# Kernel optimization log

Measured on AMD Instinct MI355X. Metric: run time of the kernel, lower is better.

## Reference

```python
import jax, jax.numpy as jnp
import numpy as np

NEG_SLOPE = 0.2  # PyG GATConv default leaky_relu slope


def add_self_loops(edge_index, n):
    loop = jnp.arange(n, dtype=edge_index.dtype)
    return jnp.concatenate([edge_index, jnp.stack([loop, loop])], axis=1)


def gat_conv(x, edge_index, W, a_src, a_dst, b):
    """PyG-style GATConv: x [N,Cin], W [Cin,H*F], a_* [H,F], b [H*F]. Returns [N,H*F]."""
    N = x.shape[0]
    H, F = a_src.shape
    xw = (x @ W).reshape(N, H, F)                      # per-head projected features
    alpha_s = jnp.sum(xw * a_src, axis=-1)             # [N,H]
    alpha_d = jnp.sum(xw * a_dst, axis=-1)             # [N,H]
    src, dst = edge_index[0], edge_index[1]
    e = alpha_s[src] + alpha_d[dst]                    # [E,H]
    e = jnp.where(e > 0, e, NEG_SLOPE * e)             # leaky_relu
    # segment softmax over edges grouped by destination node
    emax = jax.ops.segment_max(e, dst, num_segments=N)
    emax = jnp.where(jnp.isfinite(emax), emax, 0.0)
    p = jnp.exp(e - emax[dst])
    denom = jax.ops.segment_sum(p, dst, num_segments=N)
    alpha = p / (denom[dst] + 1e-16)                   # [E,H]
    msg = xw[src] * alpha[:, :, None]                  # [E,H,F]
    out = jax.ops.segment_sum(msg, dst, num_segments=N)  # [N,H,F]
    return out.reshape(N, H * F) + b


def setup_inputs() -> dict:
    key = jax.random.key(0)
    ks = jax.random.split(key, 10)
    N, E, FEAT, HID, HEADS = 50000, 800000, 256, 64, 4
    x = jax.random.normal(ks[0], (N, FEAT), dtype=jnp.float32)
    src = jax.random.randint(ks[1], (E,), 0, N, dtype=jnp.int64)
    dst = jax.random.randint(ks[2], (E,), 0, N, dtype=jnp.int64)
    dst = jnp.where(src == dst, (dst + 1) % N, dst)  # no pre-existing self loops
    edge_index = jnp.stack([src, dst])
    s1 = 1.0 / np.sqrt(FEAT)
    s2 = 1.0 / np.sqrt(HID * HEADS)
    return {
        "x": x,
        "edge_index": edge_index,
        "w1": jax.random.normal(ks[3], (FEAT, HEADS * HID), dtype=jnp.float32) * s1,
        "a_src1": jax.random.normal(ks[4], (HEADS, HID), dtype=jnp.float32) * 0.1,
        "a_dst1": jax.random.normal(ks[5], (HEADS, HID), dtype=jnp.float32) * 0.1,
        "b1": jnp.zeros((HEADS * HID,), dtype=jnp.float32),
        "w2": jax.random.normal(ks[6], (HEADS * HID, 1), dtype=jnp.float32) * s2,
        "a_src2": jax.random.normal(ks[7], (1, 1), dtype=jnp.float32) * 0.1,
        "a_dst2": jax.random.normal(ks[8], (1, 1), dtype=jnp.float32) * 0.1,
        "b2": jnp.zeros((1,), dtype=jnp.float32),
    }


def reference(x, edge_index, w1, a_src1, a_dst1, b1, w2, a_src2, a_dst2, b2):
    N = x.shape[0]
    ei = add_self_loops(edge_index, N)
    h = gat_conv(x, ei, w1, a_src1, a_dst1, b1)
    h = jax.nn.relu(h)  # dropout is identity in eval mode
    return gat_conv(h, ei, w2, a_src2, a_dst2, b2)
```

## Files before the change

kernel.cpp:

```cpp
#include <hip/hip_runtime.h>
#include <cstdint>
#include <cstddef>

#define NEG_SLOPE 0.2f
#define CAP 64

typedef _Float16 f16x4 __attribute__((ext_vector_type(4)));
typedef _Float16 f16x8 __attribute__((ext_vector_type(8)));
typedef float    f32x4 __attribute__((ext_vector_type(4)));

static __device__ __forceinline__ float leaky(float x){ return x > 0.f ? x : NEG_SLOPE*x; }
static __device__ __forceinline__ unsigned fkey(float f){
  unsigned u = __float_as_uint(f);
  return (u & 0x80000000u) ? ~u : (u | 0x80000000u);
}
static __device__ __forceinline__ float fdecode(unsigned k){
  return __uint_as_float((k & 0x80000000u) ? (k ^ 0x80000000u) : ~k);
}

__global__ __launch_bounds__(256) void k_setup(const unsigned int* __restrict__ w, int E,
                                               int* __restrict__ flag, unsigned* __restrict__ gkey,
                                               const float* __restrict__ W, _Float16* __restrict__ Bp,
                                               int* __restrict__ cnt, int N){
  int bid = blockIdx.x, tid = threadIdx.x;
  if (bid == 0){
    __shared__ int s;
    if (tid == 0) s = 0;
    if (tid < 8) gkey[tid] = 0u;
    __syncthreads();
    int nz = 0;
    long long total = 2LL * E;
    #pragma unroll
    for (int j = 0; j < 8; ++j){
      long long idx = ((long long)(tid * 8 + j) * total) / 2048;
      idx |= 1;
      if (idx < total) nz |= (w[idx] != 0u);
    }
    if (__any(nz) && (tid & 63) == 0) atomicOr(&s, 1);
    __syncthreads();
    if (tid == 0) *flag = s;
  } else if (bid <= 256){
    int c = bid - 1;
    int k = tid;
    float v = W[k*256 + c];
    int nb   = c >> 4;
    int frow = c & 15;
    int ks   = k >> 5;
    int kg   = (k >> 3) & 3;
    int ke   = k & 7;
    size_t idx = ((size_t)((nb*8 + ks)*64 + kg*16 + frow) << 3) + ke;
    Bp[idx] = (_Float16)v;
  } else {
    int base = (bid - 257)*1024 + tid*4;
    #pragma unroll
    for (int j = 0; j < 4; ++j){
      int idx = base + j;
      if (idx < N) cnt[idx] = 0;
    }
  }
}

__global__ __launch_bounds__(256) void k_gemm_scatter(const float* __restrict__ A,
                                                      const _Float16* __restrict__ Bp,
                                                      const float* __restrict__ a_src,
                                                      const float* __restrict__ a_dst,
                                                      _Float16* __restrict__ xw16,
                                                      float* __restrict__ as1, float* __restrict__ ad1,
                                                      int M,
                                                      const void* __restrict__ ei, int E,
                                                      const int* __restrict__ flag,
                                                      int* __restrict__ cnt,
                                                      unsigned short* __restrict__ bucket){
  __shared__ _Float16 As[64*256];
  int bid = blockIdx.x, tid = threadIdx.x;
  int g = bid >> 1;

  if (bid & 1){
    int base = g*1024 + tid;
    bool is32 = (*flag != 0);
    #pragma unroll
    for (int j = 0; j < 4; ++j){
      int i = base + j*256;
      if (i < E){
        int s, d;
        if (is32){
          const int* p = (const int*)ei;
          s = p[i]; d = p[E+i];
        } else {
          const long long* p = (const long long*)ei;
          s = (int)p[i]; d = (int)p[E+i];
        }
        int pos = atomicAdd(&cnt[d], 1);
        if (pos < CAP) bucket[(size_t)d*CAP + pos] = (unsigned short)s;
      }
    }
    return;
  }

  int bm = g * 64;
  int lane = tid & 63, wv = tid >> 6;

  {
    #pragma unroll
    for (int jj = 0; jj < 16; ++jj){
      int rr = wv*16 + jj;
      int gr = bm + rr;
      float4 v = (gr < M) ? *(const float4*)&A[(size_t)gr*256 + lane*4]
                          : make_float4(0.f,0.f,0.f,0.f);
      f16x4 h;
      h[0]=(_Float16)v.x; h[1]=(_Float16)v.y; h[2]=(_Float16)v.z; h[3]=(_Float16)v.w;
      int boff = (lane << 3) ^ ((rr & 7) << 4);
      *(f16x4*)((char*)As + rr*512 + boff) = h;
    }
  }
  __syncthreads();

  int frow = lane & 15;
  int kg   = lane >> 4;

  f32x4 acc[4][4];
  #pragma unroll
  for (int mi=0;mi<4;++mi)
    #pragma unroll
    for (int ni=0;ni<4;++ni) acc[mi][ni] = (f32x4){0.f,0.f,0.f,0.f};

  const _Float16* Bw = Bp + (((size_t)(wv*4)*8) << 9) + ((size_t)lane << 3);
  auto bload = [&](int ks, int ni)->f16x8 {
    return *(const f16x8*)(Bw + (((size_t)(ni*8 + ks)) << 9));
  };

  f16x8 b0[4], b1v[4], b2[4];
  #pragma unroll
  for (int ni=0;ni<4;++ni) b0[ni] = bload(0, ni);
  #pragma unroll
  for (int ni=0;ni<4;++ni) b1v[ni] = bload(1, ni);

  #pragma unroll
  for (int ks = 0; ks < 8; ++ks){
    if (ks < 6){
      #pragma unroll
      for (int ni=0;ni<4;++ni) b2[ni] = bload(ks+2, ni);
    }
    f16x8 a[4];
    #pragma unroll
    for (int mi=0;mi<4;++mi){
      int row = mi*16 + frow;
      int boff = (row*512 + ks*64 + kg*16) ^ ((row & 7) << 4);
      a[mi] = *(const f16x8*)((const char*)As + boff);
    }
    #pragma unroll
    for (int ni=0;ni<4;++ni)
      #pragma unroll
      for (int mi=0;mi<4;++mi)
        acc[mi][ni] = __builtin_amdgcn_mfma_f32_16x16x32_f16(a[mi], b0[ni], acc[mi][ni], 0,0,0);
    #pragma unroll
    for (int ni=0;ni<4;++ni){ b0[ni] = b1v[ni]; b1v[ni] = b2[ni]; }
  }

  float sa[4], da[4];
  #pragma unroll
  for (int ni=0;ni<4;++ni){
    sa[ni] = a_src[wv*64 + ni*16 + frow];
    da[ni] = a_dst[wv*64 + ni*16 + frow];
  }
  #pragma unroll
  for (int mi=0;mi<4;++mi){
    #pragma unroll
    for (int reg=0;reg<4;++reg){
      int row = bm + mi*16 + kg*4 + reg;
      bool ok = row < M;
      f16x4 hv4;
      hv4[0] = (_Float16)acc[mi][0][reg];
      hv4[1] = (_Float16)acc[mi][1][reg];
      hv4[2] = (_Float16)acc[mi][2][reg];
      hv4[3] = (_Float16)acc[mi][3][reg];
      if (ok) *(f16x4*)&xw16[(size_t)row*256 + wv*64 + frow*4] = hv4;
      float s = 0.f, d = 0.f;
      #pragma unroll
      for (int ni=0;ni<4;++ni){
        float fv = (float)hv4[ni];
        s = fmaf(fv, sa[ni], s);
        d = fmaf(fv, da[ni], d);
      }
      s += __shfl_xor(s, 1); d += __shfl_xor(d, 1);
      s += __shfl_xor(s, 2); d += __shfl_xor(d, 2);
      s += __shfl_xor(s, 4); d += __shfl_xor(d, 4);
      s += __shfl_xor(s, 8); d += __shfl_xor(d, 8);
      if (ok && frow == 0){
        as1[row*4 + wv] = s;
        ad1[row*4 + wv] = d;
      }
    }
  }
}

__global__ __launch_bounds__(256) void k_maxas(const float* __restrict__ as1,
                                               unsigned* __restrict__ gkey, int N){
  __shared__ float red[4][4];
  int tid = threadIdx.x, lane = tid & 63, wave = tid >> 6;
  float4 m = make_float4(-1e30f,-1e30f,-1e30f,-1e30f);
  for (int n = blockIdx.x*256 + tid; n < N; n += gridDim.x*256){
    float4 v = *(const float4*)&as1[(size_t)n*4];
    m.x = fmaxf(m.x, v.x); m.y = fmaxf(m.y, v.y);
    m.z = fmaxf(m.z, v.z); m.w = fmaxf(m.w, v.w);
  }
  #pragma unroll
  for (int off = 1; off < 64; off <<= 1){
    m.x = fmaxf(m.x, __shfl_xor(m.x, off));
    m.y = fmaxf(m.y, __shfl_xor(m.y, off));
    m.z = fmaxf(m.z, __shfl_xor(m.z, off));
    m.w = fmaxf(m.w, __shfl_xor(m.w, off));
  }
  if (lane == 0){ red[wave][0]=m.x; red[wave][1]=m.y; red[wave][2]=m.z; red[wave][3]=m.w; }
  __syncthreads();
  if (tid == 0){
    #pragma unroll
    for (int h=0; h<4; ++h){
      float v = fmaxf(fmaxf(red[0][h], red[1][h]), fmaxf(red[2][h], red[3][h]));
      atomicMax(&gkey[h], fkey(v));
    }
  }
}

__global__ __launch_bounds__(256) void k_agg1(const int* __restrict__ cnt,
                                              const unsigned short* __restrict__ bucket,
                                              const float* __restrict__ as1, const float* __restrict__ ad1,
                                              const unsigned* __restrict__ gkey,
                                              const _Float16* __restrict__ xw16, const float* __restrict__ b1,
                                              const float* __restrict__ w2,
                                              float* __restrict__ z, int N){
  int wave = threadIdx.x >> 6, lane = threadIdx.x & 63;
  int n = blockIdx.x*4 + wave;
  if (n >= N) return;
  int hd = lane >> 4;
  int fr = lane & 15;
  float ad_h  = ad1[n*4 + hd];
  float as_n  = as1[n*4 + hd];
  float Mh = leaky(fdecode(gkey[hd]) + ad_h);
  float p = __expf(leaky(as_n + ad_h) - Mh);
  float denom = p;
  f16x4 sv = *(const f16x4*)&xw16[(size_t)n*256 + lane*4];
  float4 acc;
  acc.x = p*(float)sv[0]; acc.y = p*(float)sv[1]; acc.z = p*(float)sv[2]; acc.w = p*(float)sv[3];
  int cn = __builtin_amdgcn_readfirstlane(cnt[n]);
  if (cn > CAP) cn = CAP;
  const unsigned short* bk = bucket + (size_t)n*CAP;
  int i = 0;
  for (; i + 4 <= cn; i += 4){
    ushort4 sq = *(const ushort4*)&bk[i];
    int s0 = sq.x, s1 = sq.y, s2 = sq.z, s3 = sq.w;
    f16x4 w0 = *(const f16x4*)&xw16[(size_t)s0*256 + lane*4];
    f16x4 w1 = *(const f16x4*)&xw16[(size_t)s1*256 + lane*4];
    f16x4 w2v= *(const f16x4*)&xw16[(size_t)s2*256 + lane*4];
    f16x4 w3 = *(const f16x4*)&xw16[(size_t)s3*256 + lane*4];
    float a0 = as1[s0*4 + hd];
    float a1 = as1[s1*4 + hd];
    float a2 = as1[s2*4 + hd];
    float a3 = as1[s3*4 + hd];
    float p0 = __expf(leaky(a0 + ad_h) - Mh);
    float p1 = __expf(leaky(a1 + ad_h) - Mh);
    float p2 = __expf(leaky(a2 + ad_h) - Mh);
    float p3 = __expf(leaky(a3 + ad_h) - Mh);
    denom += (p0 + p1) + (p2 + p3);
    acc.x = fmaf(p3,(float)w3[0], fmaf(p2,(float)w2v[0], fmaf(p1,(float)w1[0], fmaf(p0,(float)w0[0], acc.x))));
    acc.y = fmaf(p3,(float)w3[1], fmaf(p2,(float)w2v[1], fmaf(p1,(float)w1[1], fmaf(p0,(float)w0[1], acc.y))));
    acc.z = fmaf(p3,(float)w3[2], fmaf(p2,(float)w2v[2], fmaf(p1,(float)w1[2], fmaf(p0,(float)w0[2], acc.z))));
    acc.w = fmaf(p3,(float)w3[3], fmaf(p2,(float)w2v[3], fmaf(p1,(float)w1[3], fmaf(p0,(float)w0[3], acc.w))));
  }
  for (; i < cn; ++i){
    int s = bk[i];
    f16x4 w = *(const f16x4*)&xw16[(size_t)s*256 + lane*4];
    float a = as1[s*4 + hd];
    float pe = __expf(leaky(a + ad_h) - Mh);
    denom += pe;
    acc.x = fmaf(pe,(float)w[0], acc.x);
    acc.y = fmaf(pe,(float)w[1], acc.y);
    acc.z = fmaf(pe,(float)w[2], acc.z);
    acc.w = fmaf(pe,(float)w[3], acc.w);
  }
  float inv = 1.0f / (denom + 1e-16f);
  float4 bv, wv4;
  bv.x = b1[hd*64 +  0 + fr];  wv4.x = w2[hd*64 +  0 + fr];
  bv.y = b1[hd*64 + 16 + fr];  wv4.y = w2[hd*64 + 16 + fr];
  bv.z = b1[hd*64 + 32 + fr];  wv4.z = w2[hd*64 + 32 + fr];
  bv.w = b1[hd*64 + 48 + fr];  wv4.w = w2[hd*64 + 48 + fr];
  float4 o;
  o.x = fmaxf(fmaf(acc.x, inv, bv.x), 0.f);
  o.y = fmaxf(fmaf(acc.y, inv, bv.y), 0.f);
  o.z = fmaxf(fmaf(acc.z, inv, bv.z), 0.f);
  o.w = fmaxf(fmaf(acc.w, inv, bv.w), 0.f);
  float d = o.x*wv4.x + o.y*wv4.y + o.z*wv4.z + o.w*wv4.w;
  d += __shfl_xor(d, 1);
  d += __shfl_xor(d, 2);
  d += __shfl_xor(d, 4);
  d += __shfl_xor(d, 8);
  d += __shfl_xor(d, 16);
  d += __shfl_xor(d, 32);
  if (lane == 0) z[n] = d;
}

__global__ __launch_bounds__(256) void k_maxz(const float* __restrict__ z, unsigned* __restrict__ gkey,
                                              int N){
  __shared__ float smx[4], smn[4];
  int tid = threadIdx.x, lane = tid & 63, wave = tid >> 6;
  float mx = -1e30f, mn = -1e30f;
  for (int i = blockIdx.x*256 + tid; i < N; i += gridDim.x*256){
    float v = z[i];
    mx = fmaxf(mx, v);
    mn = fmaxf(mn, -v);
  }
  #pragma unroll
  for (int off=1; off<64; off<<=1){
    mx = fmaxf(mx, __shfl_xor(mx, off));
    mn = fmaxf(mn, __shfl_xor(mn, off));
  }
  if (lane == 0){ smx[wave] = mx; smn[wave] = mn; }
  __syncthreads();
  if (tid == 0){
    mx = fmaxf(fmaxf(smx[0], smx[1]), fmaxf(smx[2], smx[3]));
    mn = fmaxf(fmaxf(smn[0], smn[1]), fmaxf(smn[2], smn[3]));
    atomicMax(&gkey[4], fkey(mx));
    atomicMax(&gkey[5], fkey(mn));
  }
}

__global__ __launch_bounds__(256) void k_agg2(const int* __restrict__ cnt,
                                              const unsigned short* __restrict__ bucket,
                                              const float* __restrict__ z,
                                              const unsigned* __restrict__ gkey,
                                              const float* __restrict__ as2p, const float* __restrict__ ad2p,
                                              const float* __restrict__ b2p,
                                              float* __restrict__ out, int N){
  int wave = threadIdx.x >> 6, lane = threadIdx.x & 63;
  int n = blockIdx.x*4 + wave;
  if (n >= N) return;
  float cas = as2p[0], cad = ad2p[0], cb = b2p[0];
  float zmax = fdecode(gkey[4]);
  float zmin = -fdecode(gkey[5]);
  float zn = z[n];
  float adn = cad * zn;
  float bound = (cas >= 0.f) ? cas*zmax : cas*zmin;
  float M2 = leaky(bound + adn);
  int cn = __builtin_amdgcn_readfirstlane(cnt[n]);
  if (cn > CAP) cn = CAP;
  const unsigned short* bk = bucket + (size_t)n*CAP;
  float num = 0.f, den = 0.f;
  if (lane == 0){
    float p = __expf(leaky(cas*zn + adn) - M2);
    den = p; num = p * zn;
  }
  for (int i = lane; i < cn; i += 64){
    int s = bk[i];
    float zs = z[s];
    float p = __expf(leaky(cas*zs + adn) - M2);
    den += p;
    num = fmaf(p, zs, num);
  }
  num += __shfl_xor(num, 1);  den += __shfl_xor(den, 1);
  num += __shfl_xor(num, 2);  den += __shfl_xor(den, 2);
  num += __shfl_xor(num, 4);  den += __shfl_xor(den, 4);
  num += __shfl_xor(num, 8);  den += __shfl_xor(den, 8);
  num += __shfl_xor(num, 16); den += __shfl_xor(den, 16);
  num += __shfl_xor(num, 32); den += __shfl_xor(den, 32);
  if (lane == 0) out[n] = num / (den + 1e-16f) + cb;
}

extern "C" void kernel_launch(void* const* d_in, const int* in_sizes, int n_in,
                              void* d_out, int out_size, void* d_ws, size_t ws_size,
                              hipStream_t stream){
  const float* x    = (const float*)d_in[0];
  const void*  ei   = d_in[1];
  const float* w1   = (const float*)d_in[2];
  const float* asw1 = (const float*)d_in[3];
  const float* adw1 = (const float*)d_in[4];
  const float* b1   = (const float*)d_in[5];
  const float* w2   = (const float*)d_in[6];
  const float* as2  = (const float*)d_in[7];
  const float* ad2  = (const float*)d_in[8];
  const float* b2   = (const float*)d_in[9];
  const int N = in_sizes[0] / 256;
  const int E = in_sizes[1] / 2;
  float* out = (float*)d_out;

  char* wsb = (char*)d_ws;
  size_t off = 0;
  auto alloc = [&](size_t bytes) -> void* {
    void* p = wsb + off;
    off = (off + bytes + 255) & ~(size_t)255;
    return p;
  };
  int*            flag    = (int*)           alloc(4);
  unsigned*       gkey    = (unsigned*)      alloc(32);
  int*            cnt     = (int*)           alloc((size_t)N*4);
  unsigned short* bucket  = (unsigned short*)alloc((size_t)N*CAP*2);
  _Float16*       Bp      = (_Float16*)      alloc((size_t)256*256*2);
  _Float16*       xw16    = (_Float16*)      alloc((size_t)N*256*2);
  float*          as1     = (float*)         alloc((size_t)N*4*4);
  float*          ad1     = (float*)         alloc((size_t)N*4*4);
  float*          z       = (float*)         alloc((size_t)N*4);

  int zblks = (N + 1023) / 1024;
  k_setup<<<1 + 256 + zblks, 256, 0, stream>>>((const unsigned int*)ei, E, flag, gkey,
                                               w1, Bp, cnt, N);

  int gemmBlks = (N + 63) / 64;
  int scatBlks = (E + 1023) / 1024;
  int pairs    = (gemmBlks > scatBlks) ? gemmBlks : scatBlks;
  k_gemm_scatter<<<2*pairs, 256, 0, stream>>>(x, Bp, asw1, adw1, xw16, as1, ad1, N,
                                              ei, E, flag, cnt, bucket);

  k_maxas<<<32, 256, 0, stream>>>(as1, gkey, N);

  int gN4 = (N + 3) / 4;
  k_agg1<<<gN4, 256, 0, stream>>>(cnt, bucket, as1, ad1, gkey, xw16, b1, w2, z, N);
  k_maxz<<<32, 256, 0, stream>>>(z, gkey, N);
  k_agg2<<<gN4, 256, 0, stream>>>(cnt, bucket, z, gkey, as2, ad2, b2, out, N);
}
```

Baseline: 142.8 us.

## Pre-pack activations to fp16 MFMA layout in setup and drop LDS staging

Moves the fp32-to-fp16 conversion of x out of the GEMM kernel into the setup kernel, writing it in a pre-tiled MFMA fragment layout. The GEMM then loads A fragments straight from global memory with a register prefetch pipeline, like B, with no shared-memory staging or barrier. The aim is to free LDS and raise occupancy in the GEMM. The cost is an extra 25 MB fp16 write and read round trip through global memory, and each A fragment is now fetched by all four waves of a block.

Result: slower. 147.1 us (+3.0%).

```diff
diff --git a/kernel.cpp b/kernel.cpp
--- a/kernel.cpp
+++ b/kernel.cpp
@@ -21,7 +21,9 @@
 __global__ __launch_bounds__(256) void k_setup(const unsigned int* __restrict__ w, int E,
                                                int* __restrict__ flag, unsigned* __restrict__ gkey,
                                                const float* __restrict__ W, _Float16* __restrict__ Bp,
-                                               int* __restrict__ cnt, int N){
+                                               int* __restrict__ cnt, int N,
+                                               const float* __restrict__ A, _Float16* __restrict__ Ap,
+                                               int zblks, int M){
   int bid = blockIdx.x, tid = threadIdx.x;
   if (bid == 0){
     __shared__ int s;
@@ -50,17 +52,27 @@
     int ke   = k & 7;
     size_t idx = ((size_t)((nb*8 + ks)*64 + kg*16 + frow) << 3) + ke;
     Bp[idx] = (_Float16)v;
-  } else {
+  } else if (bid < 257 + zblks){
     int base = (bid - 257)*1024 + tid*4;
     #pragma unroll
     for (int j = 0; j < 4; ++j){
       int idx = base + j;
       if (idx < N) cnt[idx] = 0;
     }
-  }
-}
-
-__global__ __launch_bounds__(256) void k_gemm_scatter(const float* __restrict__ A,
+  } else {
+    int mt = bid - 257 - zblks;
+    int ks = tid >> 5, kg = (tid >> 3) & 3, ke = tid & 7;
+    size_t base = ((size_t)(mt*8 + ks)*64 + kg*16) << 3;
+    #pragma unroll
+    for (int j = 0; j < 16; ++j){
+      int row = mt*16 + j;
+      float v = (row < M) ? A[(size_t)row*256 + tid] : 0.f;
+      Ap[base + ((size_t)j << 3) + ke] = (_Float16)v;
+    }
+  }
+}
+
+__global__ __launch_bounds__(256) void k_gemm_scatter(const _Float16* __restrict__ Ap,
                                                       const _Float16* __restrict__ Bp,
                                                       const float* __restrict__ a_src,
                                                       const float* __restrict__ a_dst,
@@ -71,7 +83,6 @@
                                                       const int* __restrict__ flag,
                                                       int* __restrict__ cnt,
                                                       unsigned short* __restrict__ bucket){
-  __shared__ _Float16 As[64*256];
   int bid = blockIdx.x, tid = threadIdx.x;
   int g = bid >> 1;
 
@@ -99,22 +110,6 @@
 
   int bm = g * 64;
   int lane = tid & 63, wv = tid >> 6;
-
-  {
-    #pragma unroll
-    for (int jj = 0; jj < 16; ++jj){
-      int rr = wv*16 + jj;
-      int gr = bm + rr;
-      float4 v = (gr < M) ? *(const float4*)&A[(size_t)gr*256 + lane*4]
-                          : make_float4(0.f,0.f,0.f,0.f);
-      f16x4 h;
-      h[0]=(_Float16)v.x; h[1]=(_Float16)v.y; h[2]=(_Float16)v.z; h[3]=(_Float16)v.w;
-      int boff = (lane << 3) ^ ((rr & 7) << 4);
-      *(f16x4*)((char*)As + rr*512 + boff) = h;
-    }
-  }
-  __syncthreads();
-
   int frow = lane & 15;
   int kg   = lane >> 4;
 
@@ -124,37 +119,34 @@
     #pragma unroll
     for (int ni=0;ni<4;++ni) acc[mi][ni] = (f32x4){0.f,0.f,0.f,0.f};
 
+  const _Float16* Aw = Ap + (((size_t)(g*4)*8) << 9) + ((size_t)lane << 3);
   const _Float16* Bw = Bp + (((size_t)(wv*4)*8) << 9) + ((size_t)lane << 3);
+  auto aload = [&](int ks, int mi)->f16x8 {
+    return *(const f16x8*)(Aw + (((size_t)(mi*8 + ks)) << 9));
+  };
   auto bload = [&](int ks, int ni)->f16x8 {
     return *(const f16x8*)(Bw + (((size_t)(ni*8 + ks)) << 9));
   };
 
-  f16x8 b0[4], b1v[4], b2[4];
-  #pragma unroll
-  for (int ni=0;ni<4;++ni) b0[ni] = bload(0, ni);
-  #pragma unroll
-  for (int ni=0;ni<4;++ni) b1v[ni] = bload(1, ni);
+  f16x8 a0[4], a1r[4], a2[4], b0[4], b1v[4], b2[4];
+  #pragma unroll
+  for (int q=0;q<4;++q){ a0[q] = aload(0,q); b0[q] = bload(0,q); }
+  #pragma unroll
+  for (int q=0;q<4;++q){ a1r[q] = aload(1,q); b1v[q] = bload(1,q); }
 
   #pragma unroll
   for (int ks = 0; ks < 8; ++ks){
     if (ks < 6){
       #pragma unroll
-      for (int ni=0;ni<4;++ni) b2[ni] = bload(ks+2, ni);
-    }
-    f16x8 a[4];
-    #pragma unroll
-    for (int mi=0;mi<4;++mi){
-      int row = mi*16 + frow;
-      int boff = (row*512 + ks*64 + kg*16) ^ ((row & 7) << 4);
-      a[mi] = *(const f16x8*)((const char*)As + boff);
+      for (int q=0;q<4;++q){ a2[q] = aload(ks+2,q); b2[q] = bload(ks+2,q); }
     }
     #pragma unroll
     for (int ni=0;ni<4;++ni)
       #pragma unroll
       for (int mi=0;mi<4;++mi)
-        acc[mi][ni] = __builtin_amdgcn_mfma_f32_16x16x32_f16(a[mi], b0[ni], acc[mi][ni], 0,0,0);
-    #pragma unroll
-    for (int ni=0;ni<4;++ni){ b0[ni] = b1v[ni]; b1v[ni] = b2[ni]; }
+        acc[mi][ni] = __builtin_amdgcn_mfma_f32_16x16x32_f16(a0[mi], b0[ni], acc[mi][ni], 0,0,0);
+    #pragma unroll
+    for (int q=0;q<4;++q){ a0[q] = a1r[q]; a1r[q] = a2[q]; b0[q] = b1v[q]; b1v[q] = b2[q]; }
   }
 
   float sa[4], da[4];
@@ -382,6 +374,9 @@
   const int E = in_sizes[1] / 2;
   float* out = (float*)d_out;
 
+  int gemmBlks = (N + 63) / 64;
+  int nmt      = gemmBlks * 4;
+
   char* wsb = (char*)d_ws;
   size_t off = 0;
   auto alloc = [&](size_t bytes) -> void* {
@@ -394,19 +389,19 @@
   int*            cnt     = (int*)           alloc((size_t)N*4);
   unsigned short* bucket  = (unsigned short*)alloc((size_t)N*CAP*2);
   _Float16*       Bp      = (_Float16*)      alloc((size_t)256*256*2);
+  _Float16*       Ap      = (_Float16*)      alloc((size_t)nmt*8*64*8*2);
   _Float16*       xw16    = (_Float16*)      alloc((size_t)N*256*2);
   float*          as1     = (float*)         alloc((size_t)N*4*4);
   float*          ad1     = (float*)         alloc((size_t)N*4*4);
   float*          z       = (float*)         alloc((size_t)N*4);
 
   int zblks = (N + 1023) / 1024;
-  k_setup<<<1 + 256 + zblks, 256, 0, stream>>>((const unsigned int*)ei, E, flag, gkey,
-                                               w1, Bp, cnt, N);
-
-  int gemmBlks = (N + 63) / 64;
+  k_setup<<<1 + 256 + zblks + nmt, 256, 0, stream>>>((const unsigned int*)ei, E, flag, gkey,
+                                                     w1, Bp, cnt, N, x, Ap, zblks, N);
+
   int scatBlks = (E + 1023) / 1024;
   int pairs    = (gemmBlks > scatBlks) ? gemmBlks : scatBlks;
-  k_gemm_scatter<<<2*pairs, 256, 0, stream>>>(x, Bp, asw1, adw1, xw16, as1, ad1, N,
+  k_gemm_scatter<<<2*pairs, 256, 0, stream>>>(Ap, Bp, asw1, adw1, xw16, as1, ad1, N,
                                               ei, E, flag, cnt, bucket);
 
   k_maxas<<<32, 256, 0, stream>>>(as1, gkey, N);
```
